# Performance work log

Hardware: AMD Instinct MI355X
Metric: run time of the kernel (lower is better)

Reference implementation:

```python
import jax, jax.numpy as jnp
import numpy as np

DIM = 1024
HEADS = 16
B, N = 2, 2048


def setup_inputs() -> dict:
    key = jax.random.key(0)
    ks = jax.random.split(key, 10)
    s = 1.0 / np.sqrt(DIM)
    return {
        "y2_for": jax.random.normal(ks[0], (B, N, DIM), jnp.float32),
        "y2_back": jax.random.normal(ks[1], (B, N, DIM), jnp.float32),
        "Wq": jax.random.normal(ks[2], (DIM, DIM), jnp.float32) * s,
        "bq": jnp.zeros((DIM,), jnp.float32),
        "Wk": jax.random.normal(ks[3], (DIM, DIM), jnp.float32) * s,
        "bk": jnp.zeros((DIM,), jnp.float32),
        "Wv": jax.random.normal(ks[4], (DIM, DIM), jnp.float32) * s,
        "bv": jnp.zeros((DIM,), jnp.float32),
        "Wo": jax.random.normal(ks[5], (DIM, DIM), jnp.float32) * s,
        "bo": jnp.zeros((DIM,), jnp.float32),
    }


def reference(y2_for, y2_back, Wq, bq, Wk, bk, Wv, bv, Wo, bo):
    h = HEADS
    d = DIM // h
    scale = d ** -0.5
    q = y2_for @ Wq + bq                    # [b, n, dim]
    k = y2_back @ Wk + bk
    v = (y2_back + y2_for) @ Wv + bv

    def split_heads(x):
        b, n, _ = x.shape
        return x.reshape(b, n, h, d).transpose(0, 2, 1, 3)  # [b, h, n, d]

    q, k, v = split_heads(q), split_heads(k), split_heads(v)
    attn = jax.nn.softmax(jnp.einsum('bhid,bhjd->bhij', q, k) * scale, axis=-1)
    out = jnp.einsum('bhij,bhjd->bhid', attn, v)
    out = out.transpose(0, 2, 1, 3).reshape(y2_for.shape)   # [b, n, dim]
    out = out + y2_for + y2_back
    return out @ Wo + bo
```

## Files before the change

### kernel.cpp

```cpp
#include <hip/hip_runtime.h>

#define DIM 1024
#define HEADS 16
#define BB 2
#define NN 2048
#define HD 64
#define M_ROWS (BB*NN)

typedef __bf16 bf16x8 __attribute__((ext_vector_type(8)));
typedef float f32x4 __attribute__((ext_vector_type(4)));
typedef short s16x4 __attribute__((ext_vector_type(4)));

__device__ inline unsigned short f2bf(float f) {
    unsigned int u = __builtin_bit_cast(unsigned int, f);
    u += 0x7fffu + ((u >> 16) & 1u);
    return (unsigned short)(u >> 16);
}
__device__ inline bf16x8 as_bf16x8(uint4 v) {
    return __builtin_bit_cast(bf16x8, v);
}
__device__ __forceinline__ void gl_lds16(const unsigned short* g, unsigned short* l) {
    __builtin_amdgcn_global_load_lds(
        (const __attribute__((address_space(1))) unsigned int*)g,
        (__attribute__((address_space(3))) unsigned int*)l, 16, 0, 0);
}

__device__ __forceinline__ f32x4 mfma16x16x16bf16(s16x4 a, s16x4 b, f32x4 c) {
#if __has_builtin(__builtin_amdgcn_mfma_f32_16x16x16bf16_1k)
    return __builtin_amdgcn_mfma_f32_16x16x16bf16_1k(a, b, c, 0, 0, 0);
#else
    asm volatile("v_mfma_f32_16x16x16_bf16 %0, %1, %2, %0"
                 : "+v"(c) : "v"(a), "v"(b));
    return c;
#endif
}

__global__ __launch_bounds__(256) void prep_w(
    const float* __restrict__ Wq, const float* __restrict__ Wk,
    const float* __restrict__ Wv, const float* __restrict__ Wo,
    unsigned short* __restrict__ Wt_all)
{
    __shared__ float tile[32][33];
    const int m = blockIdx.z;
    const float* W = (m == 0) ? Wq : (m == 1) ? Wk : (m == 2) ? Wv : Wo;
    const int bk = blockIdx.x, bn = blockIdx.y;
    const int tx = threadIdx.x & 31, ty = threadIdx.x >> 5;

    #pragma unroll
    for (int i = 0; i < 32; i += 8)
        tile[ty + i][tx] = W[(size_t)(bk*32 + ty + i)*DIM + bn*32 + tx];
    __syncthreads();
    unsigned short* dst = Wt_all + (size_t)m * DIM * DIM;
    #pragma unroll
    for (int i = 0; i < 32; i += 8)
        dst[(size_t)(bn*32 + ty + i)*DIM + bk*32 + tx] = f2bf(tile[tx][ty + i]);
}

__global__ __launch_bounds__(256) void prep_act(
    const float* __restrict__ y2f, const float* __restrict__ y2b,
    unsigned short* __restrict__ Af, unsigned short* __restrict__ Ab,
    unsigned short* __restrict__ As)
{
    const size_t idx = ((size_t)blockIdx.x*256 + threadIdx.x) * 8;
    #pragma unroll
    for (int half = 0; half < 2; half++) {
        float4 f = *(const float4*)(y2f + idx + half*4);
        float4 b = *(const float4*)(y2b + idx + half*4);
        ushort4 of, ob, os;
        of.x = f2bf(f.x); of.y = f2bf(f.y); of.z = f2bf(f.z); of.w = f2bf(f.w);
        ob.x = f2bf(b.x); ob.y = f2bf(b.y); ob.z = f2bf(b.z); ob.w = f2bf(b.w);
        os.x = f2bf(f.x + b.x); os.y = f2bf(f.y + b.y);
        os.z = f2bf(f.z + b.z); os.w = f2bf(f.w + b.w);
        *(ushort4*)(Af + idx + half*4) = of;
        *(ushort4*)(Ab + idx + half*4) = ob;
        *(ushort4*)(As + idx + half*4) = os;
    }
}

__global__ __launch_bounds__(256) void gemm_qkv(
    const unsigned short* __restrict__ Af, const unsigned short* __restrict__ Ab,
    const unsigned short* __restrict__ As,
    const unsigned short* __restrict__ Wt_all,
    const float* __restrict__ bq, const float* __restrict__ bk,
    const float* __restrict__ bv,
    unsigned short* __restrict__ Qh, unsigned short* __restrict__ Kh,
    unsigned short* __restrict__ Vt)
{
    const int bm = blockIdx.x;
    const int mode = blockIdx.y >> 3;
    const int bn = blockIdx.y & 7;
    __shared__ __align__(16) unsigned short sA[128*32];
    __shared__ __align__(16) unsigned short sB[128*32];
    const int t = threadIdx.x;
    const int w = t >> 6, lane = t & 63, ln = lane & 15, quad = lane >> 4;
    const int wm = w >> 1, wn = w & 1;
    const unsigned short* Wt = Wt_all + (size_t)mode * (DIM*DIM);
    const unsigned short* A0 = (mode == 0) ? Af : (mode == 1) ? Ab : As;

    const int srow = lane >> 2;
    const int scol = (lane & 3) * 8;

    f32x4 acc[4][4];
    #pragma unroll
    for (int mi = 0; mi < 4; mi++)
        #pragma unroll
        for (int ni = 0; ni < 4; ni++)
            acc[mi][ni] = (f32x4){0.f, 0.f, 0.f, 0.f};

    for (int kt = 0; kt < 32; kt++) {
        __syncthreads();
        #pragma unroll
        for (int j = 0; j < 2; j++) {
            int row = w*32 + j*16;
            gl_lds16(A0 + (size_t)(bm*128 + row + srow)*DIM + kt*32 + scol,
                     &sA[row*32]);
            gl_lds16(Wt + (size_t)(bn*128 + row + srow)*DIM + kt*32 + scol,
                     &sB[row*32]);
        }
        __syncthreads();

        bf16x8 af[4], bfr[4];
        #pragma unroll
        for (int mi = 0; mi < 4; mi++)
            af[mi] = as_bf16x8(*(const uint4*)(&sA[(wm*64 + mi*16 + ln)*32 + quad*8]));
        #pragma unroll
        for (int ni = 0; ni < 4; ni++)
            bfr[ni] = as_bf16x8(*(const uint4*)(&sB[(wn*64 + ni*16 + ln)*32 + quad*8]));
        #pragma unroll
        for (int mi = 0; mi < 4; mi++)
            #pragma unroll
            for (int ni = 0; ni < 4; ni++)
                acc[mi][ni] = __builtin_amdgcn_mfma_f32_16x16x32_bf16(af[mi], bfr[ni], acc[mi][ni], 0, 0, 0);
    }

    const float* bias = (mode == 0) ? bq : (mode == 1) ? bk : bv;
    unsigned short* dst = (mode == 0) ? Qh : (mode == 1) ? Kh : Vt;
    const float sc = (mode == 0) ? 0.125f * 1.4426950408889634f : 1.0f;
    #pragma unroll
    for (int mi = 0; mi < 4; mi++) {
        #pragma unroll
        for (int r = 0; r < 4; r++) {
            int grow = bm*128 + wm*64 + mi*16 + quad*4 + r;
            int b_ = grow >> 11, n = grow & (NN - 1);
            #pragma unroll
            for (int ni = 0; ni < 4; ni++) {
                int gcol = bn*128 + wn*64 + ni*16 + ln;
                int hh = gcol >> 6, dd = gcol & 63;
                float val = (acc[mi][ni][r] + bias[gcol]) * sc;
                if (mode == 2)
                    dst[(((size_t)(b_*HEADS + hh))*HD + dd)*NN + n] = f2bf(val);
                else
                    dst[(((size_t)(b_*HEADS + hh))*NN + n)*HD + dd] = f2bf(val);
            }
        }
    }
}

__global__ __launch_bounds__(256) void gemm_out(
    const unsigned short* __restrict__ attp,
    const unsigned short* __restrict__ Wt_all,
    const float* __restrict__ bo, float* __restrict__ out)
{
    const int bm = blockIdx.x, bn = blockIdx.y;
    __shared__ __align__(16) unsigned short sA[64*32];
    __shared__ __align__(16) unsigned short sB[128*32];
    const int t = threadIdx.x;
    const int w = t >> 6, lane = t & 63, ln = lane & 15, quad = lane >> 4;
    const int wm = w >> 1, wn = w & 1;
    const unsigned short* Wt = Wt_all + (size_t)3 * (DIM*DIM);

    const int srow = lane >> 2;
    const int scol = (lane & 3) * 8;

    f32x4 acc[2][4];
    #pragma unroll
    for (int mi = 0; mi < 2; mi++)
        #pragma unroll
        for (int ni = 0; ni < 4; ni++)
            acc[mi][ni] = (f32x4){0.f, 0.f, 0.f, 0.f};

    for (int kt = 0; kt < 32; kt++) {
        __syncthreads();
        gl_lds16(attp + (size_t)(bm*64 + w*16 + srow)*DIM + kt*32 + scol,
                 &sA[(w*16)*32]);
        #pragma unroll
        for (int j = 0; j < 2; j++) {
            int row = w*32 + j*16;
            gl_lds16(Wt + (size_t)(bn*128 + row + srow)*DIM + kt*32 + scol,
                     &sB[row*32]);
        }
        __syncthreads();

        bf16x8 af[2], bfr[4];
        #pragma unroll
        for (int mi = 0; mi < 2; mi++)
            af[mi] = as_bf16x8(*(const uint4*)(&sA[(wm*32 + mi*16 + ln)*32 + quad*8]));
        #pragma unroll
        for (int ni = 0; ni < 4; ni++)
            bfr[ni] = as_bf16x8(*(const uint4*)(&sB[(wn*64 + ni*16 + ln)*32 + quad*8]));
        #pragma unroll
        for (int mi = 0; mi < 2; mi++)
            #pragma unroll
            for (int ni = 0; ni < 4; ni++)
                acc[mi][ni] = __builtin_amdgcn_mfma_f32_16x16x32_bf16(af[mi], bfr[ni], acc[mi][ni], 0, 0, 0);
    }

    #pragma unroll
    for (int mi = 0; mi < 2; mi++) {
        #pragma unroll
        for (int r = 0; r < 4; r++) {
            int grow = bm*64 + wm*32 + mi*16 + quad*4 + r;
            #pragma unroll
            for (int ni = 0; ni < 4; ni++) {
                int gcol = bn*128 + wn*64 + ni*16 + ln;
                out[(size_t)grow*DIM + gcol] = acc[mi][ni][r] + bo[gcol];
            }
        }
    }
}

__global__ __launch_bounds__(256) void attn_kernel(
    const unsigned short* __restrict__ Qh, const unsigned short* __restrict__ Kh,
    const unsigned short* __restrict__ Vt, const float* __restrict__ y2f,
    const float* __restrict__ y2b, unsigned short* __restrict__ attp)
{
    const int bh = blockIdx.x;
    const int qt = blockIdx.y;
    const int b = bh >> 4, h = bh & 15;
    const int t = threadIdx.x;
    const int w = t >> 6, lane = t & 63, ln = lane & 15, quad = lane >> 4;
    const int sw = ln & 7;
    const float EBIAS = 17.312340490667562f;

    __shared__ __align__(16) unsigned short sQ[64*64];
    __shared__ __align__(16) unsigned short sK[64*64];
    __shared__ __align__(16) unsigned short sVt[64*64];

    const unsigned short* Qb  = Qh + (size_t)bh * NN * HD + (size_t)qt * 64 * HD;
    const unsigned short* Kb  = Kh + (size_t)bh * NN * HD;
    const unsigned short* Vtb = Vt + (size_t)bh * HD * NN;

    const int rl = lane >> 3, cb = lane & 7;

    #pragma unroll
    for (int j = 0; j < 2; j++) {
        int row = w*16 + j*8 + rl;
        gl_lds16(Qb + (size_t)row*HD + ((cb ^ (row & 7))*8), &sQ[(w*16 + j*8)*64]);
    }

    float lsum = 0.f;
    f32x4 accO[4];
    #pragma unroll
    for (int di = 0; di < 4; di++) accO[di] = (f32x4){0.f, 0.f, 0.f, 0.f};

    for (int jt = 0; jt < 32; jt++) {
        __syncthreads();
        #pragma unroll
        for (int j = 0; j < 2; j++) {
            int row = w*16 + j*8 + rl;
            gl_lds16(Kb + (size_t)(jt*64 + row)*HD + ((cb ^ (row & 7))*8),
                     &sK[(w*16 + j*8)*64]);
            gl_lds16(Vtb + (size_t)row*NN + jt*64 + ((cb ^ (row & 7))*8),
                     &sVt[(w*16 + j*8)*64]);
        }
        __syncthreads();

        f32x4 accS[4];
        #pragma unroll
        for (int ni = 0; ni < 4; ni++) accS[ni] = (f32x4){0.f, 0.f, 0.f, 0.f};
        #pragma unroll
        for (int k0 = 0; k0 < 64; k0 += 32) {
            int blkq = (k0 >> 3) + quad;
            bf16x8 aq = as_bf16x8(*(const uint4*)(&sQ[(w*16 + ln)*64 + ((blkq ^ sw)*8)]));
            #pragma unroll
            for (int ni = 0; ni < 4; ni++) {
                bf16x8 bk = as_bf16x8(*(const uint4*)(&sK[(ni*16 + ln)*64 + ((blkq ^ sw)*8)]));
                accS[ni] = __builtin_amdgcn_mfma_f32_16x16x32_bf16(bk, aq, accS[ni], 0, 0, 0);
            }
        }

        s16x4 pf[4];
        #pragma unroll
        for (int ni = 0; ni < 4; ni++) {
            float e0 = __builtin_amdgcn_exp2f(accS[ni][0] - EBIAS);
            float e1 = __builtin_amdgcn_exp2f(accS[ni][1] - EBIAS);
            float e2 = __builtin_amdgcn_exp2f(accS[ni][2] - EBIAS);
            float e3 = __builtin_amdgcn_exp2f(accS[ni][3] - EBIAS);
            lsum += (e0 + e1) + (e2 + e3);
            unsigned int lo = (__builtin_bit_cast(unsigned int, e1) & 0xFFFF0000u)
                            | (__builtin_bit_cast(unsigned int, e0) >> 16);
            unsigned int hi = (__builtin_bit_cast(unsigned int, e3) & 0xFFFF0000u)
                            | (__builtin_bit_cast(unsigned int, e2) >> 16);
            pf[ni] = __builtin_bit_cast(s16x4, uint2{lo, hi});
        }

        #pragma unroll
        for (int ni = 0; ni < 4; ni++) {
            int blkv = 2*ni + (quad >> 1);
            int off = (quad & 1) * 4;
            #pragma unroll
            for (int di = 0; di < 4; di++) {
                s16x4 bv = __builtin_bit_cast(s16x4,
                    *(const uint2*)(&sVt[(di*16 + ln)*64 + ((blkv ^ sw)*8) + off]));
                accO[di] = mfma16x16x16bf16(pf[ni], bv, accO[di]);
            }
        }
    }

    float L = lsum;
    L += __shfl_xor(L, 16, 64);
    L += __shfl_xor(L, 32, 64);
    #pragma unroll
    for (int r = 0; r < 4; r++) {
        float Lr = __shfl(L, quad*4 + r, 64);
        float inv = 1.f / Lr;
        int n = qt*64 + w*16 + quad*4 + r;
        #pragma unroll
        for (int di = 0; di < 4; di++) {
            int c = h*64 + di*16 + ln;
            size_t gi = ((size_t)b*NN + n)*DIM + c;
            float o = accO[di][r]*inv + y2f[gi] + y2b[gi];
            attp[gi] = f2bf(o);
        }
    }
}

extern "C" void kernel_launch(void* const* d_in, const int* in_sizes, int n_in,
                              void* d_out, int out_size, void* d_ws, size_t ws_size,
                              hipStream_t stream) {
    const float* y2f = (const float*)d_in[0];
    const float* y2b = (const float*)d_in[1];
    const float* Wq  = (const float*)d_in[2];
    const float* bq  = (const float*)d_in[3];
    const float* Wk  = (const float*)d_in[4];
    const float* bk  = (const float*)d_in[5];
    const float* Wv  = (const float*)d_in[6];
    const float* bv  = (const float*)d_in[7];
    const float* Wo  = (const float*)d_in[8];
    const float* bo  = (const float*)d_in[9];
    float* out = (float*)d_out;

    const size_t NACT = (size_t)M_ROWS * DIM;
    unsigned short* ws   = (unsigned short*)d_ws;
    unsigned short* Af   = ws;
    unsigned short* Ab   = ws + NACT;
    unsigned short* As   = ws + 2*NACT;
    unsigned short* Qh   = ws + 3*NACT;
    unsigned short* Kh   = ws + 4*NACT;
    unsigned short* Vt   = ws + 5*NACT;
    unsigned short* Wt   = ws + 6*NACT;
    unsigned short* attp = Ab;

    prep_w<<<dim3(32, 32, 4), 256, 0, stream>>>(Wq, Wk, Wv, Wo, Wt);
    prep_act<<<dim3(2048), 256, 0, stream>>>(y2f, y2b, Af, Ab, As);
    gemm_qkv<<<dim3(32, 24), 256, 0, stream>>>(
        Af, Ab, As, Wt, bq, bk, bv, Qh, Kh, Vt);
    attn_kernel<<<dim3(32, 32), 256, 0, stream>>>(Qh, Kh, Vt, y2f, y2b, attp);
    gemm_out<<<dim3(64, 8), 256, 0, stream>>>(attp, Wt, bo, out);
}
```

Baseline: 226.8 us.

## Widen attention KV tiles to 128, compute row sums via MFMA, read bf16 residual

The attention kernel now loads 128-key K/V tiles per iteration, which halves the number of barrier-separated iterations. Q fragments are hoisted into registers once instead of being reloaded from LDS each tile. The softmax denominator is accumulated with an MFMA against a ones vector rather than scalar adds and shuffles, and bf16 packing uses v_perm. The residual add reads the precomputed bf16 sum As instead of two fp32 tensors, which cuts global traffic but rounds the residual to bf16.

```diff
diff --git a/kernel.cpp b/kernel.cpp
--- a/kernel.cpp
+++ b/kernel.cpp
@@ -15,6 +15,9 @@
     unsigned int u = __builtin_bit_cast(unsigned int, f);
     u += 0x7fffu + ((u >> 16) & 1u);
     return (unsigned short)(u >> 16);
+}
+__device__ inline float bf2f(unsigned short u) {
+    return __builtin_bit_cast(float, (unsigned int)u << 16);
 }
 __device__ inline bf16x8 as_bf16x8(uint4 v) {
     return __builtin_bit_cast(bf16x8, v);
@@ -221,8 +224,8 @@
 
 __global__ __launch_bounds__(256) void attn_kernel(
     const unsigned short* __restrict__ Qh, const unsigned short* __restrict__ Kh,
-    const unsigned short* __restrict__ Vt, const float* __restrict__ y2f,
-    const float* __restrict__ y2b, unsigned short* __restrict__ attp)
+    const unsigned short* __restrict__ Vt, const unsigned short* __restrict__ As,
+    unsigned short* __restrict__ attp)
 {
     const int bh = blockIdx.x;
     const int qt = blockIdx.y;
@@ -233,93 +236,109 @@
     const float EBIAS = 17.312340490667562f;
 
     __shared__ __align__(16) unsigned short sQ[64*64];
-    __shared__ __align__(16) unsigned short sK[64*64];
-    __shared__ __align__(16) unsigned short sVt[64*64];
+    __shared__ __align__(16) unsigned short sK[128*64];
+    __shared__ __align__(16) unsigned short sVt[64*128];
 
     const unsigned short* Qb  = Qh + (size_t)bh * NN * HD + (size_t)qt * 64 * HD;
     const unsigned short* Kb  = Kh + (size_t)bh * NN * HD;
     const unsigned short* Vtb = Vt + (size_t)bh * HD * NN;
 
-    const int rl = lane >> 3, cb = lane & 7;
-
-    #pragma unroll
-    for (int j = 0; j < 2; j++) {
-        int row = w*16 + j*8 + rl;
-        gl_lds16(Qb + (size_t)row*HD + ((cb ^ (row & 7))*8), &sQ[(w*16 + j*8)*64]);
-    }
-
-    float lsum = 0.f;
-    f32x4 accO[4];
-    #pragma unroll
-    for (int di = 0; di < 4; di++) accO[di] = (f32x4){0.f, 0.f, 0.f, 0.f};
-
-    for (int jt = 0; jt < 32; jt++) {
-        __syncthreads();
+    {
+        const int rl = lane >> 3, cb = lane & 7;
         #pragma unroll
         for (int j = 0; j < 2; j++) {
             int row = w*16 + j*8 + rl;
-            gl_lds16(Kb + (size_t)(jt*64 + row)*HD + ((cb ^ (row & 7))*8),
-                     &sK[(w*16 + j*8)*64]);
-            gl_lds16(Vtb + (size_t)row*NN + jt*64 + ((cb ^ (row & 7))*8),
-                     &sVt[(w*16 + j*8)*64]);
-        }
-        __syncthreads();
-
-        f32x4 accS[4];
-        #pragma unroll
-        for (int ni = 0; ni < 4; ni++) accS[ni] = (f32x4){0.f, 0.f, 0.f, 0.f};
-        #pragma unroll
-        for (int k0 = 0; k0 < 64; k0 += 32) {
-            int blkq = (k0 >> 3) + quad;
-            bf16x8 aq = as_bf16x8(*(const uint4*)(&sQ[(w*16 + ln)*64 + ((blkq ^ sw)*8)]));
-            #pragma unroll
-            for (int ni = 0; ni < 4; ni++) {
-                bf16x8 bk = as_bf16x8(*(const uint4*)(&sK[(ni*16 + ln)*64 + ((blkq ^ sw)*8)]));
-                accS[ni] = __builtin_amdgcn_mfma_f32_16x16x32_bf16(bk, aq, accS[ni], 0, 0, 0);
-            }
-        }
-
-        s16x4 pf[4];
-        #pragma unroll
-        for (int ni = 0; ni < 4; ni++) {
-            float e0 = __builtin_amdgcn_exp2f(accS[ni][0] - EBIAS);
-            float e1 = __builtin_amdgcn_exp2f(accS[ni][1] - EBIAS);
-            float e2 = __builtin_amdgcn_exp2f(accS[ni][2] - EBIAS);
-            float e3 = __builtin_amdgcn_exp2f(accS[ni][3] - EBIAS);
-            lsum += (e0 + e1) + (e2 + e3);
-            unsigned int lo = (__builtin_bit_cast(unsigned int, e1) & 0xFFFF0000u)
-                            | (__builtin_bit_cast(unsigned int, e0) >> 16);
-            unsigned int hi = (__builtin_bit_cast(unsigned int, e3) & 0xFFFF0000u)
-                            | (__builtin_bit_cast(unsigned int, e2) >> 16);
-            pf[ni] = __builtin_bit_cast(s16x4, uint2{lo, hi});
-        }
-
-        #pragma unroll
-        for (int ni = 0; ni < 4; ni++) {
-            int blkv = 2*ni + (quad >> 1);
-            int off = (quad & 1) * 4;
-            #pragma unroll
-            for (int di = 0; di < 4; di++) {
-                s16x4 bv = __builtin_bit_cast(s16x4,
-                    *(const uint2*)(&sVt[(di*16 + ln)*64 + ((blkv ^ sw)*8) + off]));
-                accO[di] = mfma16x16x16bf16(pf[ni], bv, accO[di]);
-            }
-        }
-    }
-
-    float L = lsum;
-    L += __shfl_xor(L, 16, 64);
-    L += __shfl_xor(L, 32, 64);
+            gl_lds16(Qb + (size_t)row*HD + ((cb ^ (row & 7))*8),
+                     &sQ[(w*16 + j*8)*64]);
+        }
+    }
+    __syncthreads();
+    bf16x8 aq[2];
+    #pragma unroll
+    for (int k = 0; k < 2; k++)
+        aq[k] = as_bf16x8(*(const uint4*)(&sQ[(w*16 + ln)*64 + (((k*4 + quad) ^ sw)*8)]));
+
+    const s16x4 ones = { (short)0x3F80, (short)0x3F80, (short)0x3F80, (short)0x3F80 };
+    f32x4 accO[4], accL;
+    accL = (f32x4){0.f, 0.f, 0.f, 0.f};
+    #pragma unroll
+    for (int di = 0; di < 4; di++) accO[di] = (f32x4){0.f, 0.f, 0.f, 0.f};
+
+    for (int jt = 0; jt < 16; jt++) {
+        __syncthreads();
+        {
+            const int rl = lane >> 3, p = lane & 7;
+            #pragma unroll
+            for (int j = 0; j < 4; j++) {
+                int row = w*32 + j*8 + rl;
+                gl_lds16(Kb + (size_t)(jt*128 + row)*HD + ((p ^ (row & 7))*8),
+                         &sK[(w*32 + j*8)*64]);
+            }
+        }
+        {
+            const int rl = lane >> 4, p = lane & 15;
+            #pragma unroll
+            for (int j = 0; j < 4; j++) {
+                int d = w*16 + j*4 + rl;
+                int cb = (p & 8) | ((p & 7) ^ (d & 7));
+                gl_lds16(Vtb + (size_t)d*NN + jt*128 + cb*8,
+                         &sVt[(w*16 + j*4)*128]);
+            }
+        }
+        __syncthreads();
+
+        #pragma unroll
+        for (int g = 0; g < 2; g++) {
+            f32x4 accS[4];
+            #pragma unroll
+            for (int ni = 0; ni < 4; ni++) accS[ni] = (f32x4){0.f, 0.f, 0.f, 0.f};
+            #pragma unroll
+            for (int ni = 0; ni < 4; ni++) {
+                int nn = g*4 + ni;
+                #pragma unroll
+                for (int k = 0; k < 2; k++) {
+                    bf16x8 bk = as_bf16x8(*(const uint4*)(
+                        &sK[(nn*16 + ln)*64 + (((k*4 + quad) ^ sw)*8)]));
+                    accS[ni] = __builtin_amdgcn_mfma_f32_16x16x32_bf16(bk, aq[k], accS[ni], 0, 0, 0);
+                }
+            }
+            s16x4 pf[4];
+            #pragma unroll
+            for (int ni = 0; ni < 4; ni++) {
+                unsigned int e0 = __builtin_bit_cast(unsigned int, __builtin_amdgcn_exp2f(accS[ni][0] - EBIAS));
+                unsigned int e1 = __builtin_bit_cast(unsigned int, __builtin_amdgcn_exp2f(accS[ni][1] - EBIAS));
+                unsigned int e2 = __builtin_bit_cast(unsigned int, __builtin_amdgcn_exp2f(accS[ni][2] - EBIAS));
+                unsigned int e3 = __builtin_bit_cast(unsigned int, __builtin_amdgcn_exp2f(accS[ni][3] - EBIAS));
+                unsigned int lo = __builtin_amdgcn_perm(e1, e0, 0x07060302u);
+                unsigned int hi = __builtin_amdgcn_perm(e3, e2, 0x07060302u);
+                pf[ni] = __builtin_bit_cast(s16x4, uint2{lo, hi});
+                accL = mfma16x16x16bf16(pf[ni], ones, accL);
+            }
+            #pragma unroll
+            for (int ni = 0; ni < 4; ni++) {
+                int nn = g*4 + ni;
+                int cbase = 2*nn + (quad >> 1);
+                int p = (cbase & 8) | ((cbase & 7) ^ sw);
+                int off = (quad & 1)*4;
+                #pragma unroll
+                for (int di = 0; di < 4; di++) {
+                    s16x4 bv = __builtin_bit_cast(s16x4,
+                        *(const uint2*)(&sVt[(di*16 + ln)*128 + p*8 + off]));
+                    accO[di] = mfma16x16x16bf16(pf[ni], bv, accO[di]);
+                }
+            }
+        }
+    }
+
     #pragma unroll
     for (int r = 0; r < 4; r++) {
-        float Lr = __shfl(L, quad*4 + r, 64);
-        float inv = 1.f / Lr;
+        float inv = 1.f / accL[r];
         int n = qt*64 + w*16 + quad*4 + r;
         #pragma unroll
         for (int di = 0; di < 4; di++) {
             int c = h*64 + di*16 + ln;
             size_t gi = ((size_t)b*NN + n)*DIM + c;
-            float o = accO[di][r]*inv + y2f[gi] + y2b[gi];
+            float o = accO[di][r]*inv + bf2f(As[gi]);
             attp[gi] = f2bf(o);
         }
     }
@@ -355,6 +374,6 @@
     prep_act<<<dim3(2048), 256, 0, stream>>>(y2f, y2b, Af, Ab, As);
     gemm_qkv<<<dim3(32, 24), 256, 0, stream>>>(
         Af, Ab, As, Wt, bq, bk, bv, Qh, Kh, Vt);
-    attn_kernel<<<dim3(32, 32), 256, 0, stream>>>(Qh, Kh, Vt, y2f, y2b, attp);
+    attn_kernel<<<dim3(32, 32), 256, 0, stream>>>(Qh, Kh, Vt, As, attp);
     gemm_out<<<dim3(64, 8), 256, 0, stream>>>(attp, Wt, bo, out);
 }
```

Measured after the change: 230.5 us. No clear change (+1.6%).
